# Kernel tuning notes

Measured on AMD Instinct MI355X. Metric: run time of the kernel, lower is better.

The kernel has to match this reference:

```python
import jax, jax.numpy as jnp
import numpy as np
from jax import lax

HIDDEN = 256
HORIZON = 168  # 7 * 24


def _cell(x, h, c, Wih, Whh, bih, bhh):
    # PyTorch LSTM cell: gate order i, f, g, o
    gates = x @ Wih.T + bih + h @ Whh.T + bhh  # [B, 4*HIDDEN]
    i, f, g, o = jnp.split(gates, 4, axis=-1)
    c = jax.nn.sigmoid(f) * c + jax.nn.sigmoid(i) * jnp.tanh(g)
    h = jax.nn.sigmoid(o) * jnp.tanh(c)
    return h, c


def setup_inputs() -> dict:
    key = jax.random.key(0)
    ks = jax.random.split(key, 20)
    B, T, H = 1024, 336, HIDDEN
    s = 0.05

    def p(k, shape):
        return jax.random.normal(k, shape, dtype=jnp.float32) * s

    inp = {"x": jax.random.normal(ks[0], (B, T), dtype=jnp.float32)}
    # encoder layer 0 (input_size=1), layer 1 (input=HIDDEN)
    inp["enc_Wih0"] = p(ks[1], (4 * H, 1)); inp["enc_Whh0"] = p(ks[2], (4 * H, H))
    inp["enc_bih0"] = p(ks[3], (4 * H,)); inp["enc_bhh0"] = p(ks[4], (4 * H,))
    inp["enc_Wih1"] = p(ks[5], (4 * H, H)); inp["enc_Whh1"] = p(ks[6], (4 * H, H))
    inp["enc_bih1"] = p(ks[7], (4 * H,)); inp["enc_bhh1"] = p(ks[8], (4 * H,))
    # decoder layers
    inp["dec_Wih0"] = p(ks[9], (4 * H, 1)); inp["dec_Whh0"] = p(ks[10], (4 * H, H))
    inp["dec_bih0"] = p(ks[11], (4 * H,)); inp["dec_bhh0"] = p(ks[12], (4 * H,))
    inp["dec_Wih1"] = p(ks[13], (4 * H, H)); inp["dec_Whh1"] = p(ks[14], (4 * H, H))
    inp["dec_bih1"] = p(ks[15], (4 * H,)); inp["dec_bhh1"] = p(ks[16], (4 * H,))
    # final projection hidden -> 1
    inp["fc_W"] = p(ks[17], (1, H)); inp["fc_b"] = p(ks[18], (1,))
    return inp


def reference(x, enc_Wih0, enc_Whh0, enc_bih0, enc_bhh0,
              enc_Wih1, enc_Whh1, enc_bih1, enc_bhh1,
              dec_Wih0, dec_Whh0, dec_bih0, dec_bhh0,
              dec_Wih1, dec_Whh1, dec_bih1, dec_bhh1,
              fc_W, fc_b):
    B = x.shape[0]
    xs = x[:, :, None].transpose(1, 0, 2)  # [T, B, 1]
    z = jnp.zeros((B, HIDDEN), dtype=x.dtype)

    def enc_step(carry, xt):
        h0, c0, h1, c1 = carry
        h0, c0 = _cell(xt, h0, c0, enc_Wih0, enc_Whh0, enc_bih0, enc_bhh0)
        h1, c1 = _cell(h0, h1, c1, enc_Wih1, enc_Whh1, enc_bih1, enc_bhh1)
        return (h0, c0, h1, c1), None

    (h0, c0, h1, c1), _ = lax.scan(enc_step, (z, z, z, z), xs)

    dec_inp = x[:, -1:]  # [B, 1] last observed value

    def dec_step(carry, _):
        h0, c0, h1, c1, inp = carry
        h0, c0 = _cell(inp, h0, c0, dec_Wih0, dec_Whh0, dec_bih0, dec_bhh0)
        h1, c1 = _cell(h0, h1, c1, dec_Wih1, dec_Whh1, dec_bih1, dec_bhh1)
        pred = h1 @ fc_W.T + fc_b  # [B, 1]
        return (h0, c0, h1, c1, pred), pred

    _, preds = lax.scan(dec_step, (h0, c0, h1, c1, dec_inp), None, length=HORIZON)
    return preds[:, :, 0].T  # [B, HORIZON]
```

## Files before the change

### kernel.cpp

```cpp
#include <hip/hip_runtime.h>

#define HIDDEN 256
#define TENC 336
#define HORIZ 168
#define BSZ 1024
#define BH (BSZ*HIDDEN)

typedef _Float16 f16;
typedef f16 f16x8 __attribute__((ext_vector_type(8)));
typedef float f32x4 __attribute__((ext_vector_type(4)));
typedef unsigned int u32;
typedef unsigned long long u64;

#define H0_OFF 0
#define H1_OFF (3*BH*2)
#define PP_OFF (H1_OFF + 2*BH*2)
#define F0_OFF (PP_OFF + 2*BSZ*16*4)
#define F1_OFF (F0_OFF + 1024*64)
#define WS_TOTAL (F1_OFF + 1024*64)

#define LDS_W0  0
#define LDS_W1I 32768
#define LDS_W1H 65536
#define LDS_TR  98304
#define LDS_TOTAL (LDS_TR + 4096)

__device__ __forceinline__ float sigm(float x){ return 1.0f/(1.0f+__expf(-x)); }
__device__ __forceinline__ float tanh_f(float x){ return 2.0f/(1.0f+__expf(-2.0f*x)) - 1.0f; }

__device__ __forceinline__ u64 ald64(const void* p){
  return __hip_atomic_load((const u64*)p, __ATOMIC_RELAXED, __HIP_MEMORY_SCOPE_AGENT);
}
__device__ __forceinline__ u32 ald32(const u32* p){
  return __hip_atomic_load(p, __ATOMIC_RELAXED, __HIP_MEMORY_SCOPE_AGENT);
}
__device__ __forceinline__ float aldf(const float* p){
  return __hip_atomic_load(p, __ATOMIC_RELAXED, __HIP_MEMORY_SCOPE_AGENT);
}
__device__ __forceinline__ void ast32(u32* p, u32 v){
  __hip_atomic_store(p, v, __ATOMIC_RELAXED, __HIP_MEMORY_SCOPE_AGENT);
}
__device__ __forceinline__ void ast64(u64* p, u64 v){
  __hip_atomic_store(p, v, __ATOMIC_RELAXED, __HIP_MEMORY_SCOPE_AGENT);
}

__device__ __forceinline__ f16x8 loadWfrag(const float* W, int grow, int k){
  const float* p = W + grow*HIDDEN + k;
  float4 lo = *(const float4*)p;
  float4 hi = *(const float4*)(p+4);
  f16x8 r;
  r[0]=(f16)lo.x; r[1]=(f16)lo.y; r[2]=(f16)lo.z; r[3]=(f16)lo.w;
  r[4]=(f16)hi.x; r[5]=(f16)hi.y; r[6]=(f16)hi.z; r[7]=(f16)hi.w;
  return r;
}

__device__ __forceinline__ void pollw2(const u32* f0, u32 t0, const u32* f1, u32 t1, int lane){
  const u32* sp = nullptr; u32 tgt = 0;
  if (lane < 16){ sp = f0 + lane*64; tgt = t0; }
  else if (f1 != nullptr && lane < 32){ sp = f1 + (lane-16)*64; tgt = t1; }
  for (int it = 0; it < (1<<20); ++it){
    bool ok = (sp == nullptr) || (ald32(sp) >= tgt);
    if (__all((int)ok)) break;
    __builtin_amdgcn_s_sleep(1);
  }
}

__device__ __forceinline__ void sigw(u32* line, u32 v, int lane){
  asm volatile("s_waitcnt vmcnt(0)" ::: "memory");
  if (lane == 0) ast32(line, v);
}

__device__ __forceinline__ void loadA8n(f16x8* a, const f16* slotu, int lane){
  const int r16 = (lane & 15) * 16;
  const int h8  = ((lane >> 4) & 1) * 8;
  const int jb  = lane >> 5;
  #pragma unroll
  for (int kt=0; kt<8; ++kt){
    const f16* q = slotu + (kt*2 + jb)*256 + r16 + h8;
    union { u64 w[2]; f16x8 v; } u;
    u.w[0] = ald64(q); u.w[1] = ald64(q+4);
    a[kt] = u.v;
  }
}

__device__ __forceinline__ void mm4l(f32x4* acc, const f16x8* a, const char* WL, int lane){
  #pragma unroll
  for (int kt=0; kt<8; ++kt){
    #pragma unroll
    for (int n=0; n<4; ++n){
      f16x8 bf = *(const f16x8*)(WL + ((n*8+kt)*64 + lane)*16);
      acc[n] = __builtin_amdgcn_mfma_f32_16x16x32_f16(a[kt], bf, acc[n], 0,0,0);
    }
  }
}

__device__ __forceinline__ void cell4(const f32x4* acc, const float* b, const float* wx,
                                      const float* x4, float* c, float* h4){
  #pragma unroll
  for (int q=0; q<4; ++q){
    float pi = acc[0][q] + b[0] + x4[q]*wx[0];
    float pf = acc[1][q] + b[1] + x4[q]*wx[1];
    float pg = acc[2][q] + b[2] + x4[q]*wx[2];
    float po = acc[3][q] + b[3] + x4[q]*wx[3];
    float i = sigm(pi), f = sigm(pf), gg = tanh_f(pg), o = sigm(po);
    c[q] = f*c[q] + i*gg;
    h4[q] = o*tanh_f(c[q]);
  }
}

__device__ __forceinline__ void storeHn(f16* slotbase, int u, int j, f16* tsc,
                                        const float* h4, int hi, int d, int lane){
  #pragma unroll
  for (int q=0; q<4; ++q) tsc[(hi*4+q)*16 + d] = (f16)h4[q];
  asm volatile("s_waitcnt lgkmcnt(0)" ::: "memory");
  __builtin_amdgcn_sched_barrier(0);
  u64 v = *(const u64*)(tsc + lane*4);
  ast64((u64*)(slotbase + u*4096 + j*256 + lane*4), v);
}

struct P {
  const float *x;
  const float *eWih0,*eWhh0,*eBih0,*eBhh0,*eWih1,*eWhh1,*eBih1,*eBhh1;
  const float *dWih0,*dWhh0,*dBih0,*dBhh0,*dWih1,*dWhh1,*dBih1,*dBhh1;
  const float *fcW,*fcB;
  float* out;
  char* ws;
};

__global__ void initk(char* ws){
  u32* p = (u32*)ws;
  size_t total = (size_t)WS_TOTAL / 4;
  for (size_t k = (size_t)blockIdx.x*blockDim.x + threadIdx.x; k < total;
       k += (size_t)gridDim.x*blockDim.x) p[k] = 0u;
}

__global__ __launch_bounds__(512) void lstm_main(P p){
  const int tid  = threadIdx.x;
  const int lane = tid & 63;
  const int w    = tid >> 6;
  const int chain= w >> 2;
  const int v    = w & 3;
  const int g    = blockIdx.x & 15;
  const int j    = blockIdx.x >> 4;
  const int hi   = lane >> 4;
  const int d    = lane & 15;
  const int D    = j*16 + d;
  const int unit = g*4 + v;

  extern __shared__ __align__(16) char smem[];
  char* sW0  = smem + LDS_W0;
  char* sW1i = smem + LDS_W1I;
  char* sW1h = smem + LDS_W1H;
  f16*  tsc  = (f16*)(smem + LDS_TR) + w*256;

  f16*   h0buf = (f16*)(p.ws + H0_OFF);
  f16*   h1buf = (f16*)(p.ws + H1_OFF);
  float* ppart = (float*)(p.ws + PP_OFF);
  u32*   F0    = (u32*)(p.ws + F0_OFF);
  u32*   F1    = (u32*)(p.ws + F1_OFF);
  const u32* pF0 = F0 + ((g*16 + 0)*4 + v)*16;
  const u32* pF1 = F1 + ((g*16 + 0)*4 + v)*16;
  u32* myF0 = F0 + ((g*16 + j)*4 + v)*16;
  u32* myF1 = F1 + ((g*16 + j)*4 + v)*16;

  int rows[4];
  #pragma unroll
  for (int q=0; q<4; ++q) rows[q] = g*64 + v*16 + hi*4 + q;

  float c[4] = {0.f,0.f,0.f,0.f};
  float wx[4], b0[4];
  float fcw = 0.f, fcb = 0.f;

  if (chain == 0){
    #pragma unroll
    for (int kt=0; kt<8; ++kt)
      *(f16x8*)(sW0 + ((v*8+kt)*64 + lane)*16) =
        loadWfrag(p.eWhh0, v*256 + j*16 + d, kt*32 + 8*hi);
    #pragma unroll
    for (int n=0; n<4; ++n){
      wx[n] = p.eWih0[n*256 + D];
      b0[n] = p.eBih0[n*256 + D] + p.eBhh0[n*256 + D];
    }
  } else {
    #pragma unroll
    for (int kt=0; kt<8; ++kt){
      *(f16x8*)(sW1i + ((v*8+kt)*64 + lane)*16) =
        loadWfrag(p.eWih1, v*256 + j*16 + d, kt*32 + 8*hi);
      *(f16x8*)(sW1h + ((v*8+kt)*64 + lane)*16) =
        loadWfrag(p.eWhh1, v*256 + j*16 + d, kt*32 + 8*hi);
    }
    wx[0]=wx[1]=wx[2]=wx[3]=0.f;
    #pragma unroll
    for (int n=0; n<4; ++n)
      b0[n] = p.eBih1[n*256 + D] + p.eBhh1[n*256 + D];
  }
  __syncthreads();

  if (chain == 0){
    for (int r = 0; r < TENC; ++r){
      float x4[4];
      #pragma unroll
      for (int q=0; q<4; ++q) x4[q] = p.x[rows[q]*TENC + r];
      pollw2(pF0, (u32)r, pF1, (r>=2)?(u32)(r-2):0u, lane);
      f16x8 a[8];
      loadA8n(a, h0buf + ((r+2)%3)*BH + unit*4096, lane);
      f32x4 acc[4] = {{0,0,0,0},{0,0,0,0},{0,0,0,0},{0,0,0,0}};
      mm4l(acc, a, sW0, lane);
      float h4[4];
      cell4(acc, b0, wx, x4, c, h4);
      storeHn(h0buf + (r%3)*BH, unit, j, tsc, h4, hi, d, lane);
      sigw(myF0, (u32)(r+1), lane);
    }
  } else {
    for (int r = 0; r < TENC; ++r){
      pollw2(pF0, (u32)(r+1), pF1, (u32)r, lane);
      f16x8 a0[8], a1[8];
      loadA8n(a0, h0buf + (r%3)*BH + unit*4096, lane);
      loadA8n(a1, h1buf + ((r+1)&1)*BH + unit*4096, lane);
      f32x4 acc[4] = {{0,0,0,0},{0,0,0,0},{0,0,0,0},{0,0,0,0}};
      mm4l(acc, a0, sW1i, lane);
      mm4l(acc, a1, sW1h, lane);
      float h4[4], xz[4] = {0.f,0.f,0.f,0.f};
      cell4(acc, b0, wx, xz, c, h4);
      storeHn(h1buf + (r&1)*BH, unit, j, tsc, h4, hi, d, lane);
      sigw(myF1, (u32)(r+1), lane);
    }
  }

  __syncthreads();
  if (chain == 0){
    #pragma unroll
    for (int kt=0; kt<8; ++kt)
      *(f16x8*)(sW0 + ((v*8+kt)*64 + lane)*16) =
        loadWfrag(p.dWhh0, v*256 + j*16 + d, kt*32 + 8*hi);
    #pragma unroll
    for (int n=0; n<4; ++n){
      wx[n] = p.dWih0[n*256 + D];
      b0[n] = p.dBih0[n*256 + D] + p.dBhh0[n*256 + D];
    }
    fcb = p.fcB[0];
  } else {
    #pragma unroll
    for (int kt=0; kt<8; ++kt){
      *(f16x8*)(sW1i + ((v*8+kt)*64 + lane)*16) =
        loadWfrag(p.dWih1, v*256 + j*16 + d, kt*32 + 8*hi);
      *(f16x8*)(sW1h + ((v*8+kt)*64 + lane)*16) =
        loadWfrag(p.dWhh1, v*256 + j*16 + d, kt*32 + 8*hi);
    }
    #pragma unroll
    for (int n=0; n<4; ++n)
      b0[n] = p.dBih1[n*256 + D] + p.dBhh1[n*256 + D];
    fcw = p.fcW[D];
  }
  __syncthreads();

  if (chain == 0){
    for (int t = 0; t < HORIZ; ++t){
      float inp4[4];
      if (t == 0){
        #pragma unroll
        for (int q=0; q<4; ++q) inp4[q] = p.x[rows[q]*TENC + (TENC-1)];
      }
      pollw2(pF0, (u32)(336+t), pF1, (t==0)?335u:(u32)(336+t), lane);
      if (t > 0){
        float pp4[4];
        #pragma unroll
        for (int q=0; q<4; ++q) pp4[q] = aldf(ppart + ((t-1)&1)*BSZ*16 + rows[q]*16 + d);
        #pragma unroll
        for (int q=0; q<4; ++q){
          float s = pp4[q];
          s += __shfl_xor(s, 1); s += __shfl_xor(s, 2);
          s += __shfl_xor(s, 4); s += __shfl_xor(s, 8);
          inp4[q] = s + fcb;
        }
      }
      f16x8 a[8];
      loadA8n(a, h0buf + ((335+t)%3)*BH + unit*4096, lane);
      f32x4 acc[4] = {{0,0,0,0},{0,0,0,0},{0,0,0,0},{0,0,0,0}};
      mm4l(acc, a, sW0, lane);
      float h4[4];
      cell4(acc, b0, wx, inp4, c, h4);
      storeHn(h0buf + ((336+t)%3)*BH, unit, j, tsc, h4, hi, d, lane);
      if (t > 0 && j == 0 && d == 0){
        #pragma unroll
        for (int q=0; q<4; ++q) p.out[rows[q]*HORIZ + (t-1)] = inp4[q];
      }
      sigw(myF0, (u32)(337+t), lane);
    }
    if (j == 0){
      pollw2(pF1, 504u, nullptr, 0, lane);
      #pragma unroll
      for (int q=0; q<4; ++q){
        float s = aldf(ppart + (167&1)*BSZ*16 + rows[q]*16 + d);
        s += __shfl_xor(s, 1); s += __shfl_xor(s, 2);
        s += __shfl_xor(s, 4); s += __shfl_xor(s, 8);
        if (d == 0) p.out[rows[q]*HORIZ + (HORIZ-1)] = s + fcb;
      }
    }
  } else {
    for (int t = 0; t < HORIZ; ++t){
      pollw2(pF0, (u32)(337+t), pF1, (u32)(336+t), lane);
      f16x8 a0[8], a1[8];
      loadA8n(a0, h0buf + ((336+t)%3)*BH + unit*4096, lane);
      loadA8n(a1, h1buf + ((t+1)&1)*BH + unit*4096, lane);
      f32x4 acc[4] = {{0,0,0,0},{0,0,0,0},{0,0,0,0},{0,0,0,0}};
      mm4l(acc, a0, sW1i, lane);
      mm4l(acc, a1, sW1h, lane);
      float h4[4], xz[4] = {0.f,0.f,0.f,0.f};
      cell4(acc, b0, wx, xz, c, h4);
      storeHn(h1buf + (t&1)*BH, unit, j, tsc, h4, hi, d, lane);
      #pragma unroll
      for (int q=0; q<4; ++q){
        float s = fcw * h4[q];
        s += __shfl_xor(s, 1); s += __shfl_xor(s, 2);
        s += __shfl_xor(s, 4); s += __shfl_xor(s, 8);
        if (d == 0)
          ast32((u32*)(ppart + (t&1)*BSZ*16 + rows[q]*16 + j), __builtin_bit_cast(u32, s));
      }
      sigw(myF1, (u32)(337+t), lane);
    }
  }
}

extern "C" void kernel_launch(void* const* d_in, const int* in_sizes, int n_in,
                              void* d_out, int out_size, void* d_ws, size_t ws_size,
                              hipStream_t stream) {
  (void)in_sizes; (void)n_in; (void)out_size;
  if (ws_size < (size_t)WS_TOTAL) return;

  P prm;
  prm.x     = (const float*)d_in[0];
  prm.eWih0 = (const float*)d_in[1];  prm.eWhh0 = (const float*)d_in[2];
  prm.eBih0 = (const float*)d_in[3];  prm.eBhh0 = (const float*)d_in[4];
  prm.eWih1 = (const float*)d_in[5];  prm.eWhh1 = (const float*)d_in[6];
  prm.eBih1 = (const float*)d_in[7];  prm.eBhh1 = (const float*)d_in[8];
  prm.dWih0 = (const float*)d_in[9];  prm.dWhh0 = (const float*)d_in[10];
  prm.dBih0 = (const float*)d_in[11]; prm.dBhh0 = (const float*)d_in[12];
  prm.dWih1 = (const float*)d_in[13]; prm.dWhh1 = (const float*)d_in[14];
  prm.dBih1 = (const float*)d_in[15]; prm.dBhh1 = (const float*)d_in[16];
  prm.fcW   = (const float*)d_in[17]; prm.fcB   = (const float*)d_in[18];
  prm.out   = (float*)d_out;
  prm.ws    = (char*)d_ws;

  hipLaunchKernelGGL(initk, dim3(256), dim3(256), 0, stream, (char*)d_ws);

  hipFuncSetAttribute((const void*)lstm_main,
                      hipFuncAttributeMaxDynamicSharedMemorySize, LDS_TOTAL);
  void* args[] = { &prm };
  hipLaunchCooperativeKernel((const void*)lstm_main, dim3(256), dim3(512),
                             args, LDS_TOTAL, stream);
}
```

Before: 4.003 ms.

## Use sc0-scoped global loads/stores for inter-block exchange with runtime coherence probe

Adds a fast path that replaces agent-scope atomic loads and stores for flags, hidden-state exchange and partial sums with plain global loads and stores carrying the sc0 cache bit, plus wide dwordx4 loads for the A fragments. A startup handshake between the 16 blocks of each group checks that sc0 traffic is visible across them, and a global vote enables the fast path only if every block passes. This aims to cut the latency of each recurrent step's cross-block communication. The risk is that visibility depends on blocks sharing a cache level (e.g. the same XCD), so the probe may fail and fall back, or pass spuriously and give incorrect results.

Result: slower. 4.356 ms (+8.8%).

```diff
diff --git a/kernel.cpp b/kernel.cpp
--- a/kernel.cpp
+++ b/kernel.cpp
@@ -10,6 +10,7 @@
 typedef f16 f16x8 __attribute__((ext_vector_type(8)));
 typedef float f32x4 __attribute__((ext_vector_type(4)));
 typedef unsigned int u32;
+typedef u32 u32x4 __attribute__((ext_vector_type(4)));
 typedef unsigned long long u64;
 
 #define H0_OFF 0
@@ -17,7 +18,9 @@
 #define PP_OFF (H1_OFF + 2*BH*2)
 #define F0_OFF (PP_OFF + 2*BSZ*16*4)
 #define F1_OFF (F0_OFF + 1024*64)
-#define WS_TOTAL (F1_OFF + 1024*64)
+#define PR_OFF (F1_OFF + 1024*64)
+#define VT_OFF (PR_OFF + 256*64)
+#define WS_TOTAL (VT_OFF + 256*64)
 
 #define LDS_W0  0
 #define LDS_W1I 32768
@@ -42,6 +45,19 @@
 }
 __device__ __forceinline__ void ast64(u64* p, u64 v){
   __hip_atomic_store(p, v, __ATOMIC_RELAXED, __HIP_MEMORY_SCOPE_AGENT);
+}
+
+__device__ __forceinline__ void st32f(u32* p, u32 v){
+  asm volatile("global_store_dword %0, %1, off sc0" :: "v"(p), "v"(v) : "memory");
+}
+__device__ __forceinline__ void st64f(u64* p, u64 v){
+  asm volatile("global_store_dwordx2 %0, %1, off sc0" :: "v"(p), "v"(v) : "memory");
+}
+__device__ __forceinline__ u32 ld32f(const u32* p){
+  u32 r;
+  asm volatile("global_load_dword %0, %1, off sc0\n\ts_waitcnt vmcnt(0)"
+               : "=v"(r) : "v"(p) : "memory");
+  return r;
 }
 
 __device__ __forceinline__ f16x8 loadWfrag(const float* W, int grow, int k){
@@ -54,32 +70,47 @@
   return r;
 }
 
-__device__ __forceinline__ void pollw2(const u32* f0, u32 t0, const u32* f1, u32 t1, int lane){
+__device__ __forceinline__ void pollw2(const u32* f0, u32 t0, const u32* f1, u32 t1,
+                                       int lane, bool fast){
   const u32* sp = nullptr; u32 tgt = 0;
   if (lane < 16){ sp = f0 + lane*64; tgt = t0; }
   else if (f1 != nullptr && lane < 32){ sp = f1 + (lane-16)*64; tgt = t1; }
   for (int it = 0; it < (1<<20); ++it){
-    bool ok = (sp == nullptr) || (ald32(sp) >= tgt);
-    if (__all((int)ok)) break;
+    u32 v = 0xffffffffu;
+    if (sp) v = fast ? ld32f(sp) : ald32(sp);
+    if (__all((int)(v >= tgt))) break;
     __builtin_amdgcn_s_sleep(1);
   }
 }
 
-__device__ __forceinline__ void sigw(u32* line, u32 v, int lane){
+__device__ __forceinline__ void sigw(u32* line, u32 v, int lane, bool fast){
   asm volatile("s_waitcnt vmcnt(0)" ::: "memory");
-  if (lane == 0) ast32(line, v);
-}
-
-__device__ __forceinline__ void loadA8n(f16x8* a, const f16* slotu, int lane){
+  if (lane == 0){ if (fast) st32f(line, v); else ast32(line, v); }
+}
+
+__device__ __forceinline__ void loadA8n(f16x8* a, const f16* slotu, int lane, bool fast){
   const int r16 = (lane & 15) * 16;
   const int h8  = ((lane >> 4) & 1) * 8;
   const int jb  = lane >> 5;
-  #pragma unroll
-  for (int kt=0; kt<8; ++kt){
-    const f16* q = slotu + (kt*2 + jb)*256 + r16 + h8;
-    union { u64 w[2]; f16x8 v; } u;
-    u.w[0] = ald64(q); u.w[1] = ald64(q+4);
-    a[kt] = u.v;
+  if (fast){
+    u32x4 r[8];
+    #pragma unroll
+    for (int kt=0; kt<8; ++kt){
+      const f16* q = slotu + (kt*2 + jb)*256 + r16 + h8;
+      asm volatile("global_load_dwordx4 %0, %1, off sc0" : "=v"(r[kt]) : "v"(q) : "memory");
+    }
+    asm volatile("s_waitcnt vmcnt(0)" ::: "memory");
+    __builtin_amdgcn_sched_barrier(0);
+    #pragma unroll
+    for (int kt=0; kt<8; ++kt) a[kt] = __builtin_bit_cast(f16x8, r[kt]);
+  } else {
+    #pragma unroll
+    for (int kt=0; kt<8; ++kt){
+      const f16* q = slotu + (kt*2 + jb)*256 + r16 + h8;
+      union { u64 w[2]; f16x8 v; } u;
+      u.w[0] = ald64(q); u.w[1] = ald64(q+4);
+      a[kt] = u.v;
+    }
   }
 }
 
@@ -109,13 +140,33 @@
 }
 
 __device__ __forceinline__ void storeHn(f16* slotbase, int u, int j, f16* tsc,
-                                        const float* h4, int hi, int d, int lane){
+                                        const float* h4, int hi, int d, int lane, bool fast){
   #pragma unroll
   for (int q=0; q<4; ++q) tsc[(hi*4+q)*16 + d] = (f16)h4[q];
   asm volatile("s_waitcnt lgkmcnt(0)" ::: "memory");
   __builtin_amdgcn_sched_barrier(0);
   u64 v = *(const u64*)(tsc + lane*4);
-  ast64((u64*)(slotbase + u*4096 + j*256 + lane*4), v);
+  u64* ad = (u64*)(slotbase + u*4096 + j*256 + lane*4);
+  if (fast) st64f(ad, v); else ast64(ad, v);
+}
+
+__device__ __forceinline__ void loadPP4(float* pp4, const float* base, const int* rows,
+                                        int d, bool fast){
+  if (fast){
+    u32 t4[4];
+    #pragma unroll
+    for (int q=0; q<4; ++q){
+      const float* ap = base + rows[q]*16 + d;
+      asm volatile("global_load_dword %0, %1, off sc0" : "=v"(t4[q]) : "v"(ap) : "memory");
+    }
+    asm volatile("s_waitcnt vmcnt(0)" ::: "memory");
+    __builtin_amdgcn_sched_barrier(0);
+    #pragma unroll
+    for (int q=0; q<4; ++q) pp4[q] = __builtin_bit_cast(float, t4[q]);
+  } else {
+    #pragma unroll
+    for (int q=0; q<4; ++q) pp4[q] = aldf(base + rows[q]*16 + d);
+  }
 }
 
 struct P {
@@ -140,8 +191,9 @@
   const int w    = tid >> 6;
   const int chain= w >> 2;
   const int v    = w & 3;
-  const int g    = blockIdx.x & 15;
-  const int j    = blockIdx.x >> 4;
+  const int blk  = blockIdx.x;
+  const int g    = blk & 15;
+  const int j    = blk >> 4;
   const int hi   = lane >> 4;
   const int d    = lane & 15;
   const int D    = j*16 + d;
@@ -152,12 +204,15 @@
   char* sW1i = smem + LDS_W1I;
   char* sW1h = smem + LDS_W1H;
   f16*  tsc  = (f16*)(smem + LDS_TR) + w*256;
+  __shared__ int sFast;
 
   f16*   h0buf = (f16*)(p.ws + H0_OFF);
   f16*   h1buf = (f16*)(p.ws + H1_OFF);
   float* ppart = (float*)(p.ws + PP_OFF);
   u32*   F0    = (u32*)(p.ws + F0_OFF);
   u32*   F1    = (u32*)(p.ws + F1_OFF);
+  u32*   PR    = (u32*)(p.ws + PR_OFF);
+  u32*   VT    = (u32*)(p.ws + VT_OFF);
   const u32* pF0 = F0 + ((g*16 + 0)*4 + v)*16;
   const u32* pF1 = F1 + ((g*16 + 0)*4 + v)*16;
   u32* myF0 = F0 + ((g*16 + j)*4 + v)*16;
@@ -194,36 +249,80 @@
     for (int n=0; n<4; ++n)
       b0[n] = p.eBih1[n*256 + D] + p.eBhh1[n*256 + D];
   }
+
+  if (w == 0){
+    u32* myP = PR + (g*16 + j)*16;
+    const u32* gP = PR + (g*16)*16;
+    const u32 mexp1 = (lane < 16) ? (0x00A50000u | (u32)((lane<<4) | g)) : 0u;
+    const u32 mexp2 = (lane < 16) ? (0x005A0000u | (u32)((lane<<4) | g)) : 0u;
+
+    st32f(myP, 0x00A50000u | (u32)blk);
+    bool ok1 = (lane >= 16);
+    if (lane < 16){
+      const u32* sp = gP + lane*16;
+      for (int it = 0; it < (1<<12); ++it){
+        if (ld32f(sp) == mexp1){ ok1 = true; break; }
+      }
+    }
+    int a1 = __all((int)ok1);
+
+    st32f(myP + 1, 0x005A0000u | (u32)blk);
+    bool ok2 = (lane >= 16);
+    if (lane < 16){
+      const u32* sp = gP + lane*16 + 1;
+      for (int it = 0; it < (1<<12); ++it){
+        if (ld32f(sp) == mexp2){ ok2 = true; break; }
+      }
+    }
+    int a2 = __all((int)ok2);
+    u32 myok = (a1 && a2) ? 1u : 0u;
+
+    ast32(VT + (g*16 + j)*16, 0x100u | myok);
+    bool vok = (lane >= 16);
+    if (lane < 16){
+      const u32* vp = VT + (g*16 + lane)*16;
+      u32 vv = 0;
+      for (int it = 0; it < (1<<20); ++it){
+        vv = ald32(vp);
+        if (vv & 0x100u) break;
+        __builtin_amdgcn_s_sleep(1);
+      }
+      vok = ((vv & 0x100u) != 0) && ((vv & 1u) != 0);
+    }
+    int allok = __all((int)vok);
+    if (lane == 0) sFast = allok;
+  }
   __syncthreads();
+  const bool fast = (sFast != 0);
 
   if (chain == 0){
     for (int r = 0; r < TENC; ++r){
       float x4[4];
       #pragma unroll
       for (int q=0; q<4; ++q) x4[q] = p.x[rows[q]*TENC + r];
-      pollw2(pF0, (u32)r, pF1, (r>=2)?(u32)(r-2):0u, lane);
+      pollw2(pF0, (u32)r, pF1, (r>=2)?(u32)(r-2):0u, lane, fast);
       f16x8 a[8];
-      loadA8n(a, h0buf + ((r+2)%3)*BH + unit*4096, lane);
+      loadA8n(a, h0buf + ((r+2)%3)*BH + unit*4096, lane, fast);
       f32x4 acc[4] = {{0,0,0,0},{0,0,0,0},{0,0,0,0},{0,0,0,0}};
       mm4l(acc, a, sW0, lane);
       float h4[4];
       cell4(acc, b0, wx, x4, c, h4);
-      storeHn(h0buf + (r%3)*BH, unit, j, tsc, h4, hi, d, lane);
-      sigw(myF0, (u32)(r+1), lane);
+      storeHn(h0buf + (r%3)*BH, unit, j, tsc, h4, hi, d, lane, fast);
+      sigw(myF0, (u32)(r+1), lane, fast);
     }
   } else {
     for (int r = 0; r < TENC; ++r){
-      pollw2(pF0, (u32)(r+1), pF1, (u32)r, lane);
+      pollw2(pF0, (u32)(r+1), pF1, (u32)r, lane, fast);
       f16x8 a0[8], a1[8];
-      loadA8n(a0, h0buf + (r%3)*BH + unit*4096, lane);
-      loadA8n(a1, h1buf + ((r+1)&1)*BH + unit*4096, lane);
+      loadA8n(a0, h0buf + (r%3)*BH + unit*4096, lane, fast);
+      loadA8n(a1, h1buf + ((r+1)&1)*BH + unit*4096, lane, fast);
       f32x4 acc[4] = {{0,0,0,0},{0,0,0,0},{0,0,0,0},{0,0,0,0}};
       mm4l(acc, a0, sW1i, lane);
       mm4l(acc, a1, sW1h, lane);
       float h4[4], xz[4] = {0.f,0.f,0.f,0.f};
       cell4(acc, b0, wx, xz, c, h4);
-      storeHn(h1buf + (r&1)*BH, unit, j, tsc, h4, hi, d, lane);
-      sigw(myF1, (u32)(r+1), lane);
+      storeHn(h1buf + (r&1)*BH, unit, j, tsc, h4, hi, d, lane, fast);
+      sigw(myF1, (u32)(r+1), lane, fast);
     }
   }
 
@@ -261,11 +360,10 @@
         #pragma unroll
         for (int q=0; q<4; ++q) inp4[q] = p.x[rows[q]*TENC + (TENC-1)];
       }
-      pollw2(pF0, (u32)(336+t), pF1, (t==0)?335u:(u32)(336+t), lane);
+      pollw2(pF0, (u32)(336+t), pF1, (t==0)?335u:(u32)(336+t), lane, fast);
       if (t > 0){
         float pp4[4];
-        #pragma unroll
-        for (int q=0; q<4; ++q) pp4[q] = aldf(ppart + ((t-1)&1)*BSZ*16 + rows[q]*16 + d);
+        loadPP4(pp4, ppart + ((t-1)&1)*BSZ*16, rows, d, fast);
         #pragma unroll
         for (int q=0; q<4; ++q){
           float s = pp4[q];
@@ -275,23 +373,25 @@
         }
       }
       f16x8 a[8];
-      loadA8n(a, h0buf + ((335+t)%3)*BH + unit*4096, lane);
+      loadA8n(a, h0buf + ((335+t)%3)*BH + unit*4096, lane, fast);
       f32x4 acc[4] = {{0,0,0,0},{0,0,0,0},{0,0,0,0},{0,0,0,0}};
       mm4l(acc, a, sW0, lane);
       float h4[4];
       cell4(acc, b0, wx, inp4, c, h4);
-      storeHn(h0buf + ((336+t)%3)*BH, unit, j, tsc, h4, hi, d, lane);
+      storeHn(h0buf + ((336+t)%3)*BH, unit, j, tsc, h4, hi, d, lane, fast);
       if (t > 0 && j == 0 && d == 0){
         #pragma unroll
         for (int q=0; q<4; ++q) p.out[rows[q]*HORIZ + (t-1)] = inp4[q];
       }
-      sigw(myF0, (u32)(337+t), lane);
+      sigw(myF0, (u32)(337+t), lane, fast);
     }
     if (j == 0){
-      pollw2(pF1, 504u, nullptr, 0, lane);
+      pollw2(pF1, 504u, nullptr, 0, lane, fast);
+      float pp4[4];
+      loadPP4(pp4, ppart + (167&1)*BSZ*16, rows, d, fast);
       #pragma unroll
       for (int q=0; q<4; ++q){
-        float s = aldf(ppart + (167&1)*BSZ*16 + rows[q]*16 + d);
+        float s = pp4[q];
         s += __shfl_xor(s, 1); s += __shfl_xor(s, 2);
         s += __shfl_xor(s, 4); s += __shfl_xor(s, 8);
         if (d == 0) p.out[rows[q]*HORIZ + (HORIZ-1)] = s + fcb;
@@ -299,25 +399,28 @@
     }
   } else {
     for (int t = 0; t < HORIZ; ++t){
-      pollw2(pF0, (u32)(337+t), pF1, (u32)(336+t), lane);
+      pollw2(pF0, (u32)(337+t), pF1, (u32)(336+t), lane, fast);
       f16x8 a0[8], a1[8];
-      loadA8n(a0, h0buf + ((336+t)%3)*BH + unit*4096, lane);
-      loadA8n(a1, h1buf + ((t+1)&1)*BH + unit*4096, lane);
+      loadA8n(a0, h0buf + ((336+t)%3)*BH + unit*4096, lane, fast);
+      loadA8n(a1, h1buf + ((t+1)&1)*BH + unit*4096, lane, fast);
       f32x4 acc[4] = {{0,0,0,0},{0,0,0,0},{0,0,0,0},{0,0,0,0}};
       mm4l(acc, a0, sW1i, lane);
       mm4l(acc, a1, sW1h, lane);
       float h4[4], xz[4] = {0.f,0.f,0.f,0.f};
       cell4(acc, b0, wx, xz, c, h4);
-      storeHn(h1buf + (t&1)*BH, unit, j, tsc, h4, hi, d, lane);
+      storeHn(h1buf + (t&1)*BH, unit, j, tsc, h4, hi, d, lane, fast);
       #pragma unroll
       for (int q=0; q<4; ++q){
         float s = fcw * h4[q];
         s += __shfl_xor(s, 1); s += __shfl_xor(s, 2);
         s += __shfl_xor(s, 4); s += __shfl_xor(s, 8);
-        if (d == 0)
-          ast32((u32*)(ppart + (t&1)*BSZ*16 + rows[q]*16 + j), __builtin_bit_cast(u32, s));
-      }
-      sigw(myF1, (u32)(337+t), lane);
+        if (d == 0){
+          u32* ap = (u32*)(ppart + (t&1)*BSZ*16 + rows[q]*16 + j);
+          u32 sv = __builtin_bit_cast(u32, s);
+          if (fast) st32f(ap, sv); else ast32(ap, sv);
+        }
+      }
+      sigw(myF1, (u32)(337+t), lane, fast);
     }
   }
 }
```

## Transpose MFMA operands, drop LDS transpose, split polls to overlap recurrent matmuls

Applied to the files above, without the earlier changes.

Swaps the MFMA operand order so each lane holds four hidden dims of one batch row. The h output can then be packed and stored straight to global memory without the LDS transpose scratch, and the fc reduction needs only two cross-lane shuffles. The layer-1 and decoder loops now wait on the flag they need first, run the matmul that is already ready (own recurrent h or the layer-0 h), and only then wait for the other dependency. This is meant to hide inter-block synchronisation latency behind MFMA work. In exchange there are more per-lane bias and weight registers and two poll loops per step.

Measured after the change: 4.365 ms. 1.09x slower.

```diff
diff --git a/kernel.cpp b/kernel.cpp
--- a/kernel.cpp
+++ b/kernel.cpp
@@ -10,6 +10,7 @@
 typedef f16 f16x8 __attribute__((ext_vector_type(8)));
 typedef float f32x4 __attribute__((ext_vector_type(4)));
 typedef unsigned int u32;
+typedef unsigned short u16;
 typedef unsigned long long u64;
 
 #define H0_OFF 0
@@ -22,8 +23,7 @@
 #define LDS_W0  0
 #define LDS_W1I 32768
 #define LDS_W1H 65536
-#define LDS_TR  98304
-#define LDS_TOTAL (LDS_TR + 4096)
+#define LDS_TOTAL 98304
 
 __device__ __forceinline__ float sigm(float x){ return 1.0f/(1.0f+__expf(-x)); }
 __device__ __forceinline__ float tanh_f(float x){ return 2.0f/(1.0f+__expf(-2.0f*x)) - 1.0f; }
@@ -32,9 +32,6 @@
   return __hip_atomic_load((const u64*)p, __ATOMIC_RELAXED, __HIP_MEMORY_SCOPE_AGENT);
 }
 __device__ __forceinline__ u32 ald32(const u32* p){
-  return __hip_atomic_load(p, __ATOMIC_RELAXED, __HIP_MEMORY_SCOPE_AGENT);
-}
-__device__ __forceinline__ float aldf(const float* p){
   return __hip_atomic_load(p, __ATOMIC_RELAXED, __HIP_MEMORY_SCOPE_AGENT);
 }
 __device__ __forceinline__ void ast32(u32* p, u32 v){
@@ -59,8 +56,9 @@
   if (lane < 16){ sp = f0 + lane*64; tgt = t0; }
   else if (f1 != nullptr && lane < 32){ sp = f1 + (lane-16)*64; tgt = t1; }
   for (int it = 0; it < (1<<20); ++it){
-    bool ok = (sp == nullptr) || (ald32(sp) >= tgt);
-    if (__all((int)ok)) break;
+    u32 v = 0xffffffffu;
+    if (sp) v = ald32(sp);
+    if (__all((int)(v >= tgt))) break;
     __builtin_amdgcn_s_sleep(1);
   }
 }
@@ -83,39 +81,40 @@
   }
 }
 
-__device__ __forceinline__ void mm4l(f32x4* acc, const f16x8* a, const char* WL, int lane){
+__device__ __forceinline__ void mm4W(f32x4* acc, const f16x8* a, const char* WL, int lane){
   #pragma unroll
   for (int kt=0; kt<8; ++kt){
     #pragma unroll
     for (int n=0; n<4; ++n){
-      f16x8 bf = *(const f16x8*)(WL + ((n*8+kt)*64 + lane)*16);
-      acc[n] = __builtin_amdgcn_mfma_f32_16x16x32_f16(a[kt], bf, acc[n], 0,0,0);
-    }
-  }
-}
-
-__device__ __forceinline__ void cell4(const f32x4* acc, const float* b, const float* wx,
-                                      const float* x4, float* c, float* h4){
+      f16x8 wf = *(const f16x8*)(WL + ((n*8+kt)*64 + lane)*16);
+      acc[n] = __builtin_amdgcn_mfma_f32_16x16x32_f16(wf, a[kt], acc[n], 0,0,0);
+    }
+  }
+}
+
+__device__ __forceinline__ void cellT(const f32x4* acc, const float bv[4][4],
+                                      const float wxv[4][4], float xr,
+                                      float* cst, float* h4){
   #pragma unroll
   for (int q=0; q<4; ++q){
-    float pi = acc[0][q] + b[0] + x4[q]*wx[0];
-    float pf = acc[1][q] + b[1] + x4[q]*wx[1];
-    float pg = acc[2][q] + b[2] + x4[q]*wx[2];
-    float po = acc[3][q] + b[3] + x4[q]*wx[3];
+    float pi = acc[0][q] + bv[0][q] + xr*wxv[0][q];
+    float pf = acc[1][q] + bv[1][q] + xr*wxv[1][q];
+    float pg = acc[2][q] + bv[2][q] + xr*wxv[2][q];
+    float po = acc[3][q] + bv[3][q] + xr*wxv[3][q];
     float i = sigm(pi), f = sigm(pf), gg = tanh_f(pg), o = sigm(po);
-    c[q] = f*c[q] + i*gg;
-    h4[q] = o*tanh_f(c[q]);
-  }
-}
-
-__device__ __forceinline__ void storeHn(f16* slotbase, int u, int j, f16* tsc,
-                                        const float* h4, int hi, int d, int lane){
+    cst[q] = f*cst[q] + i*gg;
+    h4[q] = o*tanh_f(cst[q]);
+  }
+}
+
+__device__ __forceinline__ void storeH2(f16* chunk, const float* h4, int lane){
+  u64 v = 0;
   #pragma unroll
-  for (int q=0; q<4; ++q) tsc[(hi*4+q)*16 + d] = (f16)h4[q];
-  asm volatile("s_waitcnt lgkmcnt(0)" ::: "memory");
-  __builtin_amdgcn_sched_barrier(0);
-  u64 v = *(const u64*)(tsc + lane*4);
-  ast64((u64*)(slotbase + u*4096 + j*256 + lane*4), v);
+  for (int q=0; q<4; ++q){
+    u16 b = __builtin_bit_cast(u16, (f16)h4[q]);
+    v |= (u64)b << (16*q);
+  }
+  ast64((u64*)(chunk + (lane&15)*16 + (lane>>4)*4), v);
 }
 
 struct P {
@@ -140,18 +139,17 @@
   const int w    = tid >> 6;
   const int chain= w >> 2;
   const int v    = w & 3;
-  const int g    = blockIdx.x & 15;
-  const int j    = blockIdx.x >> 4;
-  const int hi   = lane >> 4;
-  const int d    = lane & 15;
-  const int D    = j*16 + d;
+  const int blk  = blockIdx.x;
+  const int g    = blk & 15;
+  const int j    = blk >> 4;
   const int unit = g*4 + v;
+  const int row  = g*64 + v*16 + (lane & 15);
+  const int hq   = lane >> 4;
 
   extern __shared__ __align__(16) char smem[];
   char* sW0  = smem + LDS_W0;
   char* sW1i = smem + LDS_W1I;
   char* sW1h = smem + LDS_W1H;
-  f16*  tsc  = (f16*)(smem + LDS_TR) + w*256;
 
   f16*   h0buf = (f16*)(p.ws + H0_OFF);
   f16*   h1buf = (f16*)(p.ws + H1_OFF);
@@ -163,66 +161,69 @@
   u32* myF0 = F0 + ((g*16 + j)*4 + v)*16;
   u32* myF1 = F1 + ((g*16 + j)*4 + v)*16;
 
-  int rows[4];
-  #pragma unroll
-  for (int q=0; q<4; ++q) rows[q] = g*64 + v*16 + hi*4 + q;
-
-  float c[4] = {0.f,0.f,0.f,0.f};
-  float wx[4], b0[4];
-  float fcw = 0.f, fcb = 0.f;
+  float cst[4] = {0.f,0.f,0.f,0.f};
+  float bv[4][4], wxv[4][4], fcwv[4];
+  float fcb = 0.f;
 
   if (chain == 0){
     #pragma unroll
     for (int kt=0; kt<8; ++kt)
       *(f16x8*)(sW0 + ((v*8+kt)*64 + lane)*16) =
-        loadWfrag(p.eWhh0, v*256 + j*16 + d, kt*32 + 8*hi);
-    #pragma unroll
-    for (int n=0; n<4; ++n){
-      wx[n] = p.eWih0[n*256 + D];
-      b0[n] = p.eBih0[n*256 + D] + p.eBhh0[n*256 + D];
-    }
+        loadWfrag(p.eWhh0, v*256 + j*16 + (lane&15), kt*32 + 8*hq);
+    #pragma unroll
+    for (int n=0; n<4; ++n)
+      #pragma unroll
+      for (int q=0; q<4; ++q){
+        int dim = j*16 + hq*4 + q;
+        wxv[n][q] = p.eWih0[n*256 + dim];
+        bv[n][q]  = p.eBih0[n*256 + dim] + p.eBhh0[n*256 + dim];
+      }
   } else {
     #pragma unroll
     for (int kt=0; kt<8; ++kt){
       *(f16x8*)(sW1i + ((v*8+kt)*64 + lane)*16) =
-        loadWfrag(p.eWih1, v*256 + j*16 + d, kt*32 + 8*hi);
+        loadWfrag(p.eWih1, v*256 + j*16 + (lane&15), kt*32 + 8*hq);
       *(f16x8*)(sW1h + ((v*8+kt)*64 + lane)*16) =
-        loadWfrag(p.eWhh1, v*256 + j*16 + d, kt*32 + 8*hi);
-    }
-    wx[0]=wx[1]=wx[2]=wx[3]=0.f;
+        loadWfrag(p.eWhh1, v*256 + j*16 + (lane&15), kt*32 + 8*hq);
+    }
     #pragma unroll
     for (int n=0; n<4; ++n)
-      b0[n] = p.eBih1[n*256 + D] + p.eBhh1[n*256 + D];
+      #pragma unroll
+      for (int q=0; q<4; ++q){
+        int dim = j*16 + hq*4 + q;
+        wxv[n][q] = 0.f;
+        bv[n][q]  = p.eBih1[n*256 + dim] + p.eBhh1[n*256 + dim];
+      }
   }
   __syncthreads();
 
   if (chain == 0){
     for (int r = 0; r < TENC; ++r){
-      float x4[4];
-      #pragma unroll
-      for (int q=0; q<4; ++q) x4[q] = p.x[rows[q]*TENC + r];
+      float xr = p.x[row*TENC + r];
       pollw2(pF0, (u32)r, pF1, (r>=2)?(u32)(r-2):0u, lane);
       f16x8 a[8];
       loadA8n(a, h0buf + ((r+2)%3)*BH + unit*4096, lane);
       f32x4 acc[4] = {{0,0,0,0},{0,0,0,0},{0,0,0,0},{0,0,0,0}};
-      mm4l(acc, a, sW0, lane);
+      mm4W(acc, a, sW0, lane);
       float h4[4];
-      cell4(acc, b0, wx, x4, c, h4);
-      storeHn(h0buf + (r%3)*BH, unit, j, tsc, h4, hi, d, lane);
+      cellT(acc, bv, wxv, xr, cst, h4);
+      storeH2(h0buf + (r%3)*BH + unit*4096 + j*256, h4, lane);
       sigw(myF0, (u32)(r+1), lane);
     }
   } else {
     for (int r = 0; r < TENC; ++r){
-      pollw2(pF0, (u32)(r+1), pF1, (u32)r, lane);
-      f16x8 a0[8], a1[8];
-      loadA8n(a0, h0buf + (r%3)*BH + unit*4096, lane);
+      pollw2(pF1, (u32)r, nullptr, 0, lane);
+      f16x8 a1[8];
       loadA8n(a1, h1buf + ((r+1)&1)*BH + unit*4096, lane);
       f32x4 acc[4] = {{0,0,0,0},{0,0,0,0},{0,0,0,0},{0,0,0,0}};
-      mm4l(acc, a0, sW1i, lane);
-      mm4l(acc, a1, sW1h, lane);
-      float h4[4], xz[4] = {0.f,0.f,0.f,0.f};
-      cell4(acc, b0, wx, xz, c, h4);
-      storeHn(h1buf + (r&1)*BH, unit, j, tsc, h4, hi, d, lane);
+      mm4W(acc, a1, sW1h, lane);
+      pollw2(pF0, (u32)(r+1), nullptr, 0, lane);
+      f16x8 a0[8];
+      loadA8n(a0, h0buf + (r%3)*BH + unit*4096, lane);
+      mm4W(acc, a0, sW1i, lane);
+      float h4[4];
+      cellT(acc, bv, wxv, 0.f, cst, h4);
+      storeH2(h1buf + (r&1)*BH + unit*4096 + j*256, h4, lane);
       sigw(myF1, (u32)(r+1), lane);
     }
   }
@@ -232,91 +233,92 @@
     #pragma unroll
     for (int kt=0; kt<8; ++kt)
       *(f16x8*)(sW0 + ((v*8+kt)*64 + lane)*16) =
-        loadWfrag(p.dWhh0, v*256 + j*16 + d, kt*32 + 8*hi);
-    #pragma unroll
-    for (int n=0; n<4; ++n){
-      wx[n] = p.dWih0[n*256 + D];
-      b0[n] = p.dBih0[n*256 + D] + p.dBhh0[n*256 + D];
-    }
+        loadWfrag(p.dWhh0, v*256 + j*16 + (lane&15), kt*32 + 8*hq);
+    #pragma unroll
+    for (int n=0; n<4; ++n)
+      #pragma unroll
+      for (int q=0; q<4; ++q){
+        int dim = j*16 + hq*4 + q;
+        wxv[n][q] = p.dWih0[n*256 + dim];
+        bv[n][q]  = p.dBih0[n*256 + dim] + p.dBhh0[n*256 + dim];
+      }
     fcb = p.fcB[0];
   } else {
     #pragma unroll
     for (int kt=0; kt<8; ++kt){
       *(f16x8*)(sW1i + ((v*8+kt)*64 + lane)*16) =
-        loadWfrag(p.dWih1, v*256 + j*16 + d, kt*32 + 8*hi);
+        loadWfrag(p.dWih1, v*256 + j*16 + (lane&15), kt*32 + 8*hq);
       *(f16x8*)(sW1h + ((v*8+kt)*64 + lane)*16) =
-        loadWfrag(p.dWhh1, v*256 + j*16 + d, kt*32 + 8*hi);
+        loadWfrag(p.dWhh1, v*256 + j*16 + (lane&15), kt*32 + 8*hq);
     }
     #pragma unroll
     for (int n=0; n<4; ++n)
-      b0[n] = p.dBih1[n*256 + D] + p.dBhh1[n*256 + D];
-    fcw = p.fcW[D];
+      #pragma unroll
+      for (int q=0; q<4; ++q){
+        int dim = j*16 + hq*4 + q;
+        wxv[n][q] = 0.f;
+        bv[n][q]  = p.dBih1[n*256 + dim] + p.dBhh1[n*256 + dim];
+        if (n == 0) fcwv[q] = p.fcW[dim];
+      }
   }
   __syncthreads();
 
   if (chain == 0){
     for (int t = 0; t < HORIZ; ++t){
-      float inp4[4];
-      if (t == 0){
-        #pragma unroll
-        for (int q=0; q<4; ++q) inp4[q] = p.x[rows[q]*TENC + (TENC-1)];
-      }
-      pollw2(pF0, (u32)(336+t), pF1, (t==0)?335u:(u32)(336+t), lane);
-      if (t > 0){
-        float pp4[4];
-        #pragma unroll
-        for (int q=0; q<4; ++q) pp4[q] = aldf(ppart + ((t-1)&1)*BSZ*16 + rows[q]*16 + d);
-        #pragma unroll
-        for (int q=0; q<4; ++q){
-          float s = pp4[q];
-          s += __shfl_xor(s, 1); s += __shfl_xor(s, 2);
-          s += __shfl_xor(s, 4); s += __shfl_xor(s, 8);
-          inp4[q] = s + fcb;
-        }
-      }
+      pollw2(pF0, (u32)(336+t), nullptr, 0, lane);
       f16x8 a[8];
       loadA8n(a, h0buf + ((335+t)%3)*BH + unit*4096, lane);
       f32x4 acc[4] = {{0,0,0,0},{0,0,0,0},{0,0,0,0},{0,0,0,0}};
-      mm4l(acc, a, sW0, lane);
+      mm4W(acc, a, sW0, lane);
+      pollw2(pF1, (t==0)?335u:(u32)(336+t), nullptr, 0, lane);
+      float inp;
+      if (t == 0){
+        inp = p.x[row*TENC + (TENC-1)];
+      } else {
+        const float* ps = ppart + ((t-1)&1)*BSZ*16 + row*16 + hq*4;
+        u64 w0 = ald64(ps), w1 = ald64(ps+2);
+        float s = __builtin_bit_cast(float,(u32)(w0 & 0xffffffffull))
+                + __builtin_bit_cast(float,(u32)(w0 >> 32))
+                + __builtin_bit_cast(float,(u32)(w1 & 0xffffffffull))
+                + __builtin_bit_cast(float,(u32)(w1 >> 32));
+        s += __shfl_xor(s, 16); s += __shfl_xor(s, 32);
+        inp = s + fcb;
+      }
       float h4[4];
-      cell4(acc, b0, wx, inp4, c, h4);
-      storeHn(h0buf + ((336+t)%3)*BH, unit, j, tsc, h4, hi, d, lane);
-      if (t > 0 && j == 0 && d == 0){
-        #pragma unroll
-        for (int q=0; q<4; ++q) p.out[rows[q]*HORIZ + (t-1)] = inp4[q];
-      }
+      cellT(acc, bv, wxv, inp, cst, h4);
+      storeH2(h0buf + ((336+t)%3)*BH + unit*4096 + j*256, h4, lane);
+      if (t > 0 && j == 0 && lane < 16) p.out[row*HORIZ + (t-1)] = inp;
       sigw(myF0, (u32)(337+t), lane);
     }
     if (j == 0){
       pollw2(pF1, 504u, nullptr, 0, lane);
-      #pragma unroll
-      for (int q=0; q<4; ++q){
-        float s = aldf(ppart + (167&1)*BSZ*16 + rows[q]*16 + d);
-        s += __shfl_xor(s, 1); s += __shfl_xor(s, 2);
-        s += __shfl_xor(s, 4); s += __shfl_xor(s, 8);
-        if (d == 0) p.out[rows[q]*HORIZ + (HORIZ-1)] = s + fcb;
-      }
+      const float* ps = ppart + (167&1)*BSZ*16 + row*16 + hq*4;
+      u64 w0 = ald64(ps), w1 = ald64(ps+2);
+      float s = __builtin_bit_cast(float,(u32)(w0 & 0xffffffffull))
+              + __builtin_bit_cast(float,(u32)(w0 >> 32))
+              + __builtin_bit_cast(float,(u32)(w1 & 0xffffffffull))
+              + __builtin_bit_cast(float,(u32)(w1 >> 32));
+      s += __shfl_xor(s, 16); s += __shfl_xor(s, 32);
+      if (lane < 16) p.out[row*HORIZ + (HORIZ-1)] = s + fcb;
     }
   } else {
     for (int t = 0; t < HORIZ; ++t){
-      pollw2(pF0, (u32)(337+t), pF1, (u32)(336+t), lane);
-      f16x8 a0[8], a1[8];
-      loadA8n(a0, h0buf + ((336+t)%3)*BH + unit*4096, lane);
+      pollw2(pF1, (u32)(336+t), nullptr, 0, lane);
+      f16x8 a1[8];
       loadA8n(a1, h1buf + ((t+1)&1)*BH + unit*4096, lane);
       f32x4 acc[4] = {{0,0,0,0},{0,0,0,0},{0,0,0,0},{0,0,0,0}};
-      mm4l(acc, a0, sW1i, lane);
-      mm4l(acc, a1, sW1h, lane);
-      float h4[4], xz[4] = {0.f,0.f,0.f,0.f};
-      cell4(acc, b0, wx, xz, c, h4);
-      storeHn(h1buf + (t&1)*BH, unit, j, tsc, h4, hi, d, lane);
-      #pragma unroll
-      for (int q=0; q<4; ++q){
-        float s = fcw * h4[q];
-        s += __shfl_xor(s, 1); s += __shfl_xor(s, 2);
-        s += __shfl_xor(s, 4); s += __shfl_xor(s, 8);
-        if (d == 0)
-          ast32((u32*)(ppart + (t&1)*BSZ*16 + rows[q]*16 + j), __builtin_bit_cast(u32, s));
-      }
+      mm4W(acc, a1, sW1h, lane);
+      pollw2(pF0, (u32)(337+t), nullptr, 0, lane);
+      f16x8 a0[8];
+      loadA8n(a0, h0buf + ((336+t)%3)*BH + unit*4096, lane);
+      mm4W(acc, a0, sW1i, lane);
+      float h4[4];
+      cellT(acc, bv, wxv, 0.f, cst, h4);
+      storeH2(h1buf + (t&1)*BH + unit*4096 + j*256, h4, lane);
+      float s = fcwv[0]*h4[0] + fcwv[1]*h4[1] + fcwv[2]*h4[2] + fcwv[3]*h4[3];
+      s += __shfl_xor(s, 16); s += __shfl_xor(s, 32);
+      if (lane < 16)
+        ast32((u32*)(ppart + (t&1)*BSZ*16 + row*16 + j), __builtin_bit_cast(u32, s));
       sigw(myF1, (u32)(337+t), lane);
     }
   }
```
